# Kernel optimization log

Hardware: AMD Instinct MI355X
Metric: run time of the kernel (lower is better)

The kernel has to match this reference:

```python
import jax, jax.numpy as jnp
import numpy as np

N_SECTORS = 10          # = 1.0 / slice_range with normalized slice indices in [0, 1)
SLICE_RANGE = 0.1
PAIRWISE_EPS = 1e-6     # torch.nn.functional.pairwise_distance default eps (added to the diff)


def setup_inputs() -> dict:
    key = jax.random.key(0)
    k1, k2, k3, k4 = jax.random.split(key, 4)
    source_embeddings = jax.random.normal(k1, (200000, 256), dtype=jnp.float32)
    source_sectors = jax.random.randint(k2, (200000,), 0, N_SECTORS, dtype=jnp.int32)
    target_embeddings = jax.random.normal(k3, (100000, 256), dtype=jnp.float32)
    target_slice_idx = jax.random.uniform(k4, (100000,), dtype=jnp.float32)
    return {
        "source_embeddings": source_embeddings,
        "source_sectors": source_sectors,
        "target_embeddings": target_embeddings,
        "target_slice_idx": target_slice_idx,
    }


def reference(source_embeddings, source_sectors, target_embeddings, target_slice_idx):
    # cluster_centers[i] = mean of source_embeddings where source_sectors == i
    sums = jax.ops.segment_sum(source_embeddings, source_sectors, num_segments=N_SECTORS)  # [S, D]
    counts = jax.ops.segment_sum(
        jnp.ones((source_embeddings.shape[0],), dtype=source_embeddings.dtype),
        source_sectors, num_segments=N_SECTORS)                                            # [S]
    cluster_centers = sums / counts[:, None]                                               # [S, D]

    # get_sectors_from_index: bucket normalized slice index into sectors of width slice_range
    target_sectors = jnp.clip(
        jnp.floor(target_slice_idx / SLICE_RANGE).astype(jnp.int32), 0, N_SECTORS - 1)     # [N]

    cc = cluster_centers[target_sectors]                                                   # [N, D] gather

    # F.pairwise_distance with p=2, eps=1e-6: ||x1 - x2 + eps||_2
    diff = target_embeddings - cc + PAIRWISE_EPS
    distances = jnp.sqrt(jnp.sum(diff * diff, axis=-1))                                    # [N]
    return distances.mean()
```

## Files before the change

### kernel.cpp

```cpp
#include <hip/hip_runtime.h>
#include <math.h>

#define D      256
#define NSEC   10
#define EPS    1e-6f
#define SLICE  0.1f

#define WS_SUMS 0
#define WS_CNT  (NSEC * D)
#define WS_PART (NSEC * D + NSEC)
#define WS_ZERO_FLOATS (NSEC * D + NSEC)

#define DIST_BLOCKS 256

__global__ void k_zero(float* __restrict__ ws) {
    int i = blockIdx.x * blockDim.x + threadIdx.x;
    if (i < WS_ZERO_FLOATS) ws[i] = 0.f;
}

__global__ __launch_bounds__(256) void k_sums(const float* __restrict__ emb,
                                              const int* __restrict__ sec,
                                              float* __restrict__ ws, int nrows) {
    const int lane = threadIdx.x & 63;
    const int wid  = threadIdx.x >> 6;
    const int gw   = blockIdx.x * 4 + wid;
    const int nw   = gridDim.x * 4;

    float4 acc[NSEC];
    float  cnt[NSEC];
#pragma unroll
    for (int s = 0; s < NSEC; ++s) { acc[s] = make_float4(0.f, 0.f, 0.f, 0.f); cnt[s] = 0.f; }

    const float* ep = emb + (size_t)lane * 4;

    auto accum = [&](int sv, float4 v) {
        const int s = __builtin_amdgcn_readfirstlane(sv);
#pragma unroll
        for (int ss = 0; ss < NSEC; ++ss) {
            if (s == ss) {
                acc[ss].x += v.x; acc[ss].y += v.y; acc[ss].z += v.z; acc[ss].w += v.w;
                cnt[ss] += 1.f;
            }
        }
    };

    int r = gw;
    for (; r + 3 * nw < nrows; r += 4 * nw) {
        const int s0 = sec[r];
        const int s1 = sec[r + nw];
        const int s2 = sec[r + 2 * nw];
        const int s3 = sec[r + 3 * nw];
        const float4 v0 = *reinterpret_cast<const float4*>(ep + (size_t)r * D);
        const float4 v1 = *reinterpret_cast<const float4*>(ep + (size_t)(r + nw) * D);
        const float4 v2 = *reinterpret_cast<const float4*>(ep + (size_t)(r + 2 * nw) * D);
        const float4 v3 = *reinterpret_cast<const float4*>(ep + (size_t)(r + 3 * nw) * D);
        accum(s0, v0); accum(s1, v1); accum(s2, v2); accum(s3, v3);
    }
    for (; r < nrows; r += nw)
        accum(sec[r], *reinterpret_cast<const float4*>(ep + (size_t)r * D));

    __shared__ float lsum[NSEC * D];
    __shared__ float lcnt[NSEC];
    for (int i = threadIdx.x; i < NSEC * D; i += 256) lsum[i] = 0.f;
    if (threadIdx.x < NSEC) lcnt[threadIdx.x] = 0.f;
    __syncthreads();

    for (int w = 0; w < 4; ++w) {
        if (wid == w) {
#pragma unroll
            for (int ss = 0; ss < NSEC; ++ss) {
                float* p = &lsum[ss * D + lane * 4];
                p[0] += acc[ss].x; p[1] += acc[ss].y; p[2] += acc[ss].z; p[3] += acc[ss].w;
                if (lane == 0) lcnt[ss] += cnt[ss];
            }
        }
        __syncthreads();
    }

#pragma unroll
    for (int ss = 0; ss < NSEC; ++ss)
        atomicAdd(&ws[WS_SUMS + ss * D + threadIdx.x], lsum[ss * D + threadIdx.x]);
    if (threadIdx.x < NSEC)
        atomicAdd(&ws[WS_CNT + threadIdx.x], lcnt[threadIdx.x]);
}

__global__ __launch_bounds__(1024, 4) void k_dist(const float* __restrict__ temb,
                                                  const float* __restrict__ tsl,
                                                  float* __restrict__ ws, int nrows) {
    __shared__ float lc[NSEC * D];
    for (int i = threadIdx.x; i < NSEC * D; i += 1024) {
        const int s = i >> 8;
        lc[i] = ws[WS_SUMS + i] / ws[WS_CNT + s];
    }
    __syncthreads();

    const int lane = threadIdx.x & 63;
    const int wid  = threadIdx.x >> 6;
    const int gw   = blockIdx.x * 16 + wid;
    const int nw   = gridDim.x * 16;

    const float* tp = temb + (size_t)lane * 4;

    float wacc = 0.f;
    int r = gw;
    for (; r + 7 * nw < nrows; r += 8 * nw) {
        float  t[8];
        float4 v[8];
#pragma unroll
        for (int k = 0; k < 8; ++k) t[k] = tsl[r + k * nw];
#pragma unroll
        for (int k = 0; k < 8; ++k)
            v[k] = *reinterpret_cast<const float4*>(tp + (size_t)(r + k * nw) * D);

        float l[8];
#pragma unroll
        for (int k = 0; k < 8; ++k) {
            int s = (int)floorf(t[k] / SLICE);
            s = s < 0 ? 0 : (s > NSEC - 1 ? NSEC - 1 : s);
            const float4 c = *reinterpret_cast<const float4*>(&lc[s * D + lane * 4]);
            const float dx = v[k].x - c.x + EPS;
            const float dy = v[k].y - c.y + EPS;
            const float dz = v[k].z - c.z + EPS;
            const float dw = v[k].w - c.w + EPS;
            l[k] = dx * dx + dy * dy + dz * dz + dw * dw;
        }

#pragma unroll
        for (int off = 32; off >= 1; off >>= 1) {
#pragma unroll
            for (int k = 0; k < 8; ++k) l[k] += __shfl_xor(l[k], off, 64);
        }
#pragma unroll
        for (int k = 0; k < 8; ++k) wacc += sqrtf(l[k]);
    }
    for (; r < nrows; r += nw) {
        const float si = tsl[r];
        int s = (int)floorf(si / SLICE);
        s = s < 0 ? 0 : (s > NSEC - 1 ? NSEC - 1 : s);
        const float4 vv = *reinterpret_cast<const float4*>(tp + (size_t)r * D);
        const float4 c = *reinterpret_cast<const float4*>(&lc[s * D + lane * 4]);
        const float dx = vv.x - c.x + EPS;
        const float dy = vv.y - c.y + EPS;
        const float dz = vv.z - c.z + EPS;
        const float dw = vv.w - c.w + EPS;
        float loc = dx * dx + dy * dy + dz * dz + dw * dw;
#pragma unroll
        for (int off = 32; off >= 1; off >>= 1) loc += __shfl_xor(loc, off, 64);
        wacc += sqrtf(loc);
    }

    __shared__ float wsum[16];
    if (lane == 0) wsum[wid] = wacc;
    __syncthreads();
    if (threadIdx.x == 0) {
        float t = 0.f;
#pragma unroll
        for (int k = 0; k < 16; ++k) t += wsum[k];
        ws[WS_PART + blockIdx.x] = t;
    }
}

__global__ __launch_bounds__(256) void k_final(const float* __restrict__ ws,
                                               float* __restrict__ out, float invN) {
    float v = ws[WS_PART + threadIdx.x];
#pragma unroll
    for (int off = 32; off >= 1; off >>= 1) v += __shfl_xor(v, off, 64);
    __shared__ float s4[4];
    if ((threadIdx.x & 63) == 0) s4[threadIdx.x >> 6] = v;
    __syncthreads();
    if (threadIdx.x == 0) out[0] = (s4[0] + s4[1] + s4[2] + s4[3]) * invN;
}

extern "C" void kernel_launch(void* const* d_in, const int* in_sizes, int n_in,
                              void* d_out, int out_size, void* d_ws, size_t ws_size,
                              hipStream_t stream) {
    const float* semb = (const float*)d_in[0];
    const int*   ssec = (const int*)d_in[1];
    const float* temb = (const float*)d_in[2];
    const float* tsl  = (const float*)d_in[3];
    float* ws  = (float*)d_ws;
    float* out = (float*)d_out;
    const int nS = in_sizes[1];
    const int nT = in_sizes[3];

    hipLaunchKernelGGL(k_zero, dim3((WS_ZERO_FLOATS + 255) / 256), dim3(256), 0, stream, ws);
    hipLaunchKernelGGL(k_sums, dim3(1024), dim3(256), 0, stream, semb, ssec, ws, nS);
    hipLaunchKernelGGL(k_dist, dim3(DIST_BLOCKS), dim3(1024), 0, stream, temb, tsl, ws, nT);
    hipLaunchKernelGGL(k_final, dim3(1), dim3(256), 0, stream, ws, out, 1.0f / (float)nT);
}
```

Measured before the change: 100.8 us.

## Expand squared distance algebraically and compute per-row via LDS-transposed tiles

```diff
diff --git a/kernel.cpp b/kernel.cpp
--- a/kernel.cpp
+++ b/kernel.cpp
@@ -8,10 +8,10 @@
 
 #define WS_SUMS 0
 #define WS_CNT  (NSEC * D)
-#define WS_PART (NSEC * D + NSEC)
+#define WS_CENT (NSEC * D + NSEC)
+#define WS_K    (WS_CENT + NSEC * D)
+#define WS_PART (WS_K + NSEC)
 #define WS_ZERO_FLOATS (NSEC * D + NSEC)
-
-#define DIST_BLOCKS 256
 
 __global__ void k_zero(float* __restrict__ ws) {
     int i = blockIdx.x * blockDim.x + threadIdx.x;
@@ -84,91 +84,117 @@
         atomicAdd(&ws[WS_CNT + threadIdx.x], lcnt[threadIdx.x]);
 }
 
-__global__ __launch_bounds__(1024, 4) void k_dist(const float* __restrict__ temb,
-                                                  const float* __restrict__ tsl,
-                                                  float* __restrict__ ws, int nrows) {
-    __shared__ float lc[NSEC * D];
-    for (int i = threadIdx.x; i < NSEC * D; i += 1024) {
-        const int s = i >> 8;
-        lc[i] = ws[WS_SUMS + i] / ws[WS_CNT + s];
-    }
-    __syncthreads();
-
-    const int lane = threadIdx.x & 63;
-    const int wid  = threadIdx.x >> 6;
-    const int gw   = blockIdx.x * 16 + wid;
-    const int nw   = gridDim.x * 16;
-
-    const float* tp = temb + (size_t)lane * 4;
-
-    float wacc = 0.f;
-    int r = gw;
-    for (; r + 7 * nw < nrows; r += 8 * nw) {
-        float  t[8];
-        float4 v[8];
-#pragma unroll
-        for (int k = 0; k < 8; ++k) t[k] = tsl[r + k * nw];
-#pragma unroll
-        for (int k = 0; k < 8; ++k)
-            v[k] = *reinterpret_cast<const float4*>(tp + (size_t)(r + k * nw) * D);
-
-        float l[8];
+__global__ __launch_bounds__(256) void k_centers10(float* __restrict__ ws) {
+    const int t = threadIdx.x;
+    __shared__ float inv[NSEC];
+    if (t < NSEC) inv[t] = 1.f / ws[WS_CNT + t];
+    __syncthreads();
+#pragma unroll
+    for (int s = 0; s < NSEC; ++s)
+        ws[WS_CENT + s * D + t] = ws[WS_SUMS + s * D + t] * inv[s];
+    if (t < NSEC) {
+        const float iv = inv[t];
+        float cs = 0.f, cn = 0.f;
+#pragma unroll 4
+        for (int d = 0; d < D; ++d) {
+            const float c = ws[WS_SUMS + t * D + d] * iv;
+            cs += c; cn += c * c;
+        }
+        ws[WS_K + t] = cn - 2.f * EPS * cs + (float)D * EPS * EPS;
+    }
+}
+
+__global__ __launch_bounds__(256) void k_dist_t(const float* __restrict__ temb,
+                                                const float* __restrict__ tsl,
+                                                const float* __restrict__ ws,
+                                                float* __restrict__ part, int nrows) {
+    __shared__ float tile[256 * 33];
+    __shared__ float c_lds[NSEC * 257];
+    __shared__ float K_lds[NSEC];
+    const int t = threadIdx.x;
+
+    for (int i = t; i < NSEC * D; i += 256)
+        c_lds[(i >> 8) * 257 + (i & 255)] = ws[WS_CENT + i];
+    if (t < NSEC) K_lds[t] = ws[WS_K + t];
+
+    const int base = blockIdx.x * 256;
+    const int grow = base + t;
+    const int crow = grow < nrows ? grow : nrows - 1;
+    const float si = tsl[crow];
+    int s = (int)floorf(si / SLICE);
+    s = s < 0 ? 0 : (s > NSEC - 1 ? NSEC - 1 : s);
+
+    const int lrow   = t >> 3;
+    const int lchunk = t & 7;
+
+    float4 v[8];
+#pragma unroll
+    for (int k = 0; k < 8; ++k) {
+        int rr = base + lrow + 32 * k;
+        rr = rr < nrows ? rr : nrows - 1;
+        v[k] = *reinterpret_cast<const float4*>(temb + (size_t)rr * D + lchunk * 4);
+    }
+
+    float sq = 0.f, sm = 0.f, dot = 0.f;
+#pragma unroll 1
+    for (int dt = 0; dt < 8; ++dt) {
+        __syncthreads();
 #pragma unroll
         for (int k = 0; k < 8; ++k) {
-            int s = (int)floorf(t[k] / SLICE);
-            s = s < 0 ? 0 : (s > NSEC - 1 ? NSEC - 1 : s);
-            const float4 c = *reinterpret_cast<const float4*>(&lc[s * D + lane * 4]);
-            const float dx = v[k].x - c.x + EPS;
-            const float dy = v[k].y - c.y + EPS;
-            const float dz = v[k].z - c.z + EPS;
-            const float dw = v[k].w - c.w + EPS;
-            l[k] = dx * dx + dy * dy + dz * dz + dw * dw;
-        }
-
-#pragma unroll
-        for (int off = 32; off >= 1; off >>= 1) {
-#pragma unroll
-            for (int k = 0; k < 8; ++k) l[k] += __shfl_xor(l[k], off, 64);
-        }
-#pragma unroll
-        for (int k = 0; k < 8; ++k) wacc += sqrtf(l[k]);
-    }
-    for (; r < nrows; r += nw) {
-        const float si = tsl[r];
-        int s = (int)floorf(si / SLICE);
-        s = s < 0 ? 0 : (s > NSEC - 1 ? NSEC - 1 : s);
-        const float4 vv = *reinterpret_cast<const float4*>(tp + (size_t)r * D);
-        const float4 c = *reinterpret_cast<const float4*>(&lc[s * D + lane * 4]);
-        const float dx = vv.x - c.x + EPS;
-        const float dy = vv.y - c.y + EPS;
-        const float dz = vv.z - c.z + EPS;
-        const float dw = vv.w - c.w + EPS;
-        float loc = dx * dx + dy * dy + dz * dz + dw * dw;
-#pragma unroll
-        for (int off = 32; off >= 1; off >>= 1) loc += __shfl_xor(loc, off, 64);
-        wacc += sqrtf(loc);
-    }
-
-    __shared__ float wsum[16];
-    if (lane == 0) wsum[wid] = wacc;
+            const int wr = (lrow + 32 * k) * 33 + lchunk * 4;
+            tile[wr + 0] = v[k].x; tile[wr + 1] = v[k].y;
+            tile[wr + 2] = v[k].z; tile[wr + 3] = v[k].w;
+        }
+        if (dt < 7) {
+#pragma unroll
+            for (int k = 0; k < 8; ++k) {
+                int rr = base + lrow + 32 * k;
+                rr = rr < nrows ? rr : nrows - 1;
+                v[k] = *reinterpret_cast<const float4*>(
+                    temb + (size_t)rr * D + (dt + 1) * 32 + lchunk * 4);
+            }
+        }
+        __syncthreads();
+        const float* trow = &tile[t * 33];
+        const float* crp  = &c_lds[s * 257 + dt * 32];
+#pragma unroll
+        for (int d = 0; d < 32; ++d) {
+            const float x  = trow[d];
+            const float cv = crp[d];
+            sq  = fmaf(x, x, sq);
+            sm += x;
+            dot = fmaf(x, cv, dot);
+        }
+    }
+
+    float dist = 0.f;
+    if (grow < nrows)
+        dist = sqrtf(sq + 2.f * EPS * sm - 2.f * dot + K_lds[s]);
+
+#pragma unroll
+    for (int off = 32; off >= 1; off >>= 1) dist += __shfl_xor(dist, off, 64);
+    __shared__ float ws4[4];
+    if ((t & 63) == 0) ws4[t >> 6] = dist;
+    __syncthreads();
+    if (t == 0) part[blockIdx.x] = ws4[0] + ws4[1] + ws4[2] + ws4[3];
+}
+
+__global__ __launch_bounds__(512) void k_final(const float* __restrict__ part,
+                                               float* __restrict__ out,
+                                               int nparts, float invN) {
+    float v = 0.f;
+    for (int i = threadIdx.x; i < nparts; i += 512) v += part[i];
+#pragma unroll
+    for (int off = 32; off >= 1; off >>= 1) v += __shfl_xor(v, off, 64);
+    __shared__ float s8[8];
+    if ((threadIdx.x & 63) == 0) s8[threadIdx.x >> 6] = v;
     __syncthreads();
     if (threadIdx.x == 0) {
-        float t = 0.f;
-#pragma unroll
-        for (int k = 0; k < 16; ++k) t += wsum[k];
-        ws[WS_PART + blockIdx.x] = t;
-    }
-}
-
-__global__ __launch_bounds__(256) void k_final(const float* __restrict__ ws,
-                                               float* __restrict__ out, float invN) {
-    float v = ws[WS_PART + threadIdx.x];
-#pragma unroll
-    for (int off = 32; off >= 1; off >>= 1) v += __shfl_xor(v, off, 64);
-    __shared__ float s4[4];
-    if ((threadIdx.x & 63) == 0) s4[threadIdx.x >> 6] = v;
-    __syncthreads();
-    if (threadIdx.x == 0) out[0] = (s4[0] + s4[1] + s4[2] + s4[3]) * invN;
+        float tot = 0.f;
+#pragma unroll
+        for (int k = 0; k < 8; ++k) tot += s8[k];
+        out[0] = tot * invN;
+    }
 }
 
 extern "C" void kernel_launch(void* const* d_in, const int* in_sizes, int n_in,
@@ -182,9 +208,13 @@
     float* out = (float*)d_out;
     const int nS = in_sizes[1];
     const int nT = in_sizes[3];
+    const int nb = (nT + 255) / 256;
 
     hipLaunchKernelGGL(k_zero, dim3((WS_ZERO_FLOATS + 255) / 256), dim3(256), 0, stream, ws);
     hipLaunchKernelGGL(k_sums, dim3(1024), dim3(256), 0, stream, semb, ssec, ws, nS);
-    hipLaunchKernelGGL(k_dist, dim3(DIST_BLOCKS), dim3(1024), 0, stream, temb, tsl, ws, nT);
-    hipLaunchKernelGGL(k_final, dim3(1), dim3(256), 0, stream, ws, out, 1.0f / (float)nT);
-}
+    hipLaunchKernelGGL(k_centers10, dim3(1), dim3(256), 0, stream, ws);
+    hipLaunchKernelGGL(k_dist_t, dim3(nb), dim3(256), 0, stream,
+                       temb, tsl, ws, ws + WS_PART, nT);
+    hipLaunchKernelGGL(k_final, dim3(1), dim3(512), 0, stream,
+                       ws + WS_PART, out, nb, 1.0f / (float)nT);
+}
```

Result: slower. 106.6 us (+5.7%).

## Restructure distance kernel with per-wave row groups and LDS transposed reduction

Applied to the files above, without the earlier changes.

```diff
diff --git a/kernel.cpp b/kernel.cpp
--- a/kernel.cpp
+++ b/kernel.cpp
@@ -6,12 +6,15 @@
 #define EPS    1e-6f
 #define SLICE  0.1f
 
+#define CCS    264
+#define PS     65
+#define GR     32
+
 #define WS_SUMS 0
 #define WS_CNT  (NSEC * D)
-#define WS_PART (NSEC * D + NSEC)
+#define WS_CC   (NSEC * D + NSEC)
+#define WS_PART (WS_CC + NSEC * CCS)
 #define WS_ZERO_FLOATS (NSEC * D + NSEC)
-
-#define DIST_BLOCKS 256
 
 __global__ void k_zero(float* __restrict__ ws) {
     int i = blockIdx.x * blockDim.x + threadIdx.x;
@@ -84,91 +87,105 @@
         atomicAdd(&ws[WS_CNT + threadIdx.x], lcnt[threadIdx.x]);
 }
 
-__global__ __launch_bounds__(1024, 4) void k_dist(const float* __restrict__ temb,
+__global__ __launch_bounds__(256) void k_cc(float* __restrict__ ws) {
+    const int t = threadIdx.x;
+    __shared__ float inv[NSEC];
+    if (t < NSEC) inv[t] = 1.f / ws[WS_CNT + t];
+    __syncthreads();
+#pragma unroll
+    for (int s = 0; s < NSEC; ++s)
+        ws[WS_CC + s * CCS + t] = EPS - ws[WS_SUMS + s * D + t] * inv[s];
+    if (t < CCS - D) {
+#pragma unroll
+        for (int s = 0; s < NSEC; ++s) ws[WS_CC + s * CCS + D + t] = 0.f;
+    }
+}
+
+__global__ __launch_bounds__(256, 3) void k_dist3(const float* __restrict__ temb,
                                                   const float* __restrict__ tsl,
-                                                  float* __restrict__ ws, int nrows) {
-    __shared__ float lc[NSEC * D];
-    for (int i = threadIdx.x; i < NSEC * D; i += 1024) {
-        const int s = i >> 8;
-        lc[i] = ws[WS_SUMS + i] / ws[WS_CNT + s];
-    }
-    __syncthreads();
-
-    const int lane = threadIdx.x & 63;
-    const int wid  = threadIdx.x >> 6;
-    const int gw   = blockIdx.x * 16 + wid;
-    const int nw   = gridDim.x * 16;
-
-    const float* tp = temb + (size_t)lane * 4;
-
-    float wacc = 0.f;
-    int r = gw;
-    for (; r + 7 * nw < nrows; r += 8 * nw) {
-        float  t[8];
-        float4 v[8];
-#pragma unroll
-        for (int k = 0; k < 8; ++k) t[k] = tsl[r + k * nw];
-#pragma unroll
-        for (int k = 0; k < 8; ++k)
-            v[k] = *reinterpret_cast<const float4*>(tp + (size_t)(r + k * nw) * D);
-
-        float l[8];
-#pragma unroll
-        for (int k = 0; k < 8; ++k) {
-            int s = (int)floorf(t[k] / SLICE);
-            s = s < 0 ? 0 : (s > NSEC - 1 ? NSEC - 1 : s);
-            const float4 c = *reinterpret_cast<const float4*>(&lc[s * D + lane * 4]);
-            const float dx = v[k].x - c.x + EPS;
-            const float dy = v[k].y - c.y + EPS;
-            const float dz = v[k].z - c.z + EPS;
-            const float dw = v[k].w - c.w + EPS;
-            l[k] = dx * dx + dy * dy + dz * dz + dw * dw;
-        }
-
-#pragma unroll
-        for (int off = 32; off >= 1; off >>= 1) {
-#pragma unroll
-            for (int k = 0; k < 8; ++k) l[k] += __shfl_xor(l[k], off, 64);
-        }
-#pragma unroll
-        for (int k = 0; k < 8; ++k) wacc += sqrtf(l[k]);
-    }
-    for (; r < nrows; r += nw) {
-        const float si = tsl[r];
+                                                  const float* __restrict__ ws,
+                                                  float* __restrict__ part, int nrows) {
+    __shared__ float cc[NSEC * CCS];
+    __shared__ float pl[4][GR * PS];
+    __shared__ int   sid[4][GR];
+    __shared__ float bsum[4];
+    const int t = threadIdx.x, lane = t & 63, wid = t >> 6;
+
+    for (int i = t; i < NSEC * CCS; i += 256) cc[i] = ws[WS_CC + i];
+
+    const int gbase = (blockIdx.x * 4 + wid) * GR;
+
+    if (lane < GR) {
+        int rr = gbase + lane; if (rr >= nrows) rr = nrows - 1;
+        const float si = tsl[rr];
         int s = (int)floorf(si / SLICE);
         s = s < 0 ? 0 : (s > NSEC - 1 ? NSEC - 1 : s);
-        const float4 vv = *reinterpret_cast<const float4*>(tp + (size_t)r * D);
-        const float4 c = *reinterpret_cast<const float4*>(&lc[s * D + lane * 4]);
-        const float dx = vv.x - c.x + EPS;
-        const float dy = vv.y - c.y + EPS;
-        const float dz = vv.z - c.z + EPS;
-        const float dw = vv.w - c.w + EPS;
-        float loc = dx * dx + dy * dy + dz * dz + dw * dw;
-#pragma unroll
-        for (int off = 32; off >= 1; off >>= 1) loc += __shfl_xor(loc, off, 64);
-        wacc += sqrtf(loc);
-    }
-
-    __shared__ float wsum[16];
-    if (lane == 0) wsum[wid] = wacc;
+        sid[wid][lane] = s * CCS;
+    }
+    __syncthreads();
+
+    const float* tp = temb + (size_t)lane * 4;
+    float* P = pl[wid];
+    const int* SID = sid[wid];
+
+    float4 va[8], vb[8];
+    auto LOAD = [&](float4* v, int c) {
+#pragma unroll
+        for (int k = 0; k < 8; ++k) {
+            int rr = gbase + c * 8 + k; if (rr >= nrows) rr = nrows - 1;
+            v[k] = *reinterpret_cast<const float4*>(tp + (size_t)rr * D);
+        }
+    };
+    auto COMP = [&](float4* v, int c) {
+#pragma unroll
+        for (int k = 0; k < 8; ++k) {
+            const int row = c * 8 + k;
+            const int so  = SID[row];
+            const float4 c4 = *reinterpret_cast<const float4*>(&cc[so + lane * 4]);
+            const float dx = v[k].x + c4.x;
+            const float dy = v[k].y + c4.y;
+            const float dz = v[k].z + c4.z;
+            const float dw = v[k].w + c4.w;
+            P[row * PS + lane] = dx * dx + dy * dy + dz * dz + dw * dw;
+        }
+    };
+    LOAD(va, 0); LOAD(vb, 1); COMP(va, 0);
+    LOAD(va, 2); COMP(vb, 1);
+    LOAD(vb, 3); COMP(va, 2);
+    COMP(vb, 3);
+
+    const int row = lane & 31, half = lane >> 5;
+    float a = 0.f;
+    const float* Pr = &P[row * PS + half * 32];
+#pragma unroll
+    for (int i = 0; i < 32; ++i) a += Pr[i];
+    a += __shfl_xor(a, 32, 64);
+    const int rr = gbase + row;
+    float dsum = (rr < nrows && half == 0) ? sqrtf(a) : 0.f;
+#pragma unroll
+    for (int off = 16; off >= 1; off >>= 1) dsum += __shfl_xor(dsum, off, 64);
+
+    if (lane == 0) bsum[wid] = dsum;
+    __syncthreads();
+    if (t == 0) part[blockIdx.x] = bsum[0] + bsum[1] + bsum[2] + bsum[3];
+}
+
+__global__ __launch_bounds__(1024) void k_final(const float* __restrict__ part,
+                                                float* __restrict__ out,
+                                                int nparts, float invN) {
+    float v = 0.f;
+    for (int i = threadIdx.x; i < nparts; i += 1024) v += part[i];
+#pragma unroll
+    for (int off = 32; off >= 1; off >>= 1) v += __shfl_xor(v, off, 64);
+    __shared__ float s16[16];
+    if ((threadIdx.x & 63) == 0) s16[threadIdx.x >> 6] = v;
     __syncthreads();
     if (threadIdx.x == 0) {
-        float t = 0.f;
-#pragma unroll
-        for (int k = 0; k < 16; ++k) t += wsum[k];
-        ws[WS_PART + blockIdx.x] = t;
-    }
-}
-
-__global__ __launch_bounds__(256) void k_final(const float* __restrict__ ws,
-                                               float* __restrict__ out, float invN) {
-    float v = ws[WS_PART + threadIdx.x];
-#pragma unroll
-    for (int off = 32; off >= 1; off >>= 1) v += __shfl_xor(v, off, 64);
-    __shared__ float s4[4];
-    if ((threadIdx.x & 63) == 0) s4[threadIdx.x >> 6] = v;
-    __syncthreads();
-    if (threadIdx.x == 0) out[0] = (s4[0] + s4[1] + s4[2] + s4[3]) * invN;
+        float tot = 0.f;
+#pragma unroll
+        for (int k = 0; k < 16; ++k) tot += s16[k];
+        out[0] = tot * invN;
+    }
 }
 
 extern "C" void kernel_launch(void* const* d_in, const int* in_sizes, int n_in,
@@ -182,9 +199,13 @@
     float* out = (float*)d_out;
     const int nS = in_sizes[1];
     const int nT = in_sizes[3];
+    const int nb = (nT + 127) / 128;
 
     hipLaunchKernelGGL(k_zero, dim3((WS_ZERO_FLOATS + 255) / 256), dim3(256), 0, stream, ws);
     hipLaunchKernelGGL(k_sums, dim3(1024), dim3(256), 0, stream, semb, ssec, ws, nS);
-    hipLaunchKernelGGL(k_dist, dim3(DIST_BLOCKS), dim3(1024), 0, stream, temb, tsl, ws, nT);
-    hipLaunchKernelGGL(k_final, dim3(1), dim3(256), 0, stream, ws, out, 1.0f / (float)nT);
-}
+    hipLaunchKernelGGL(k_cc, dim3(1), dim3(256), 0, stream, ws);
+    hipLaunchKernelGGL(k_dist3, dim3(nb), dim3(256), 0, stream,
+                       temb, tsl, ws, ws + WS_PART, nT);
+    hipLaunchKernelGGL(k_final, dim3(1), dim3(1024), 0, stream,
+                       ws + WS_PART, out, nb, 1.0f / (float)nT);
+}
```

After: 105.6 us. 4.7% more time.
